# Kernel tuning notes

Hardware: AMD Instinct MI355X
Metric: run time of the kernel (lower is better)

The kernel has to match this reference:

```python
import jax, jax.numpy as jnp
import numpy as np

B, T, S, L_SRC, V, H, E, AV = 16, 128, 192, 192, 30522, 768, 768, 200
L_ORG = L_SRC - 1
KEEP, DEL, STOP, PAD = 3, 4, 2, 0  # SP_IDS = [KEEP, DEL, INSERT, STOP, PAD, LEFT, RIGHT, MARK]


def lstm(x, Wih, Whh, bih, bhh):
    # x: [B, T, E] -> outputs [B, T, H]; PyTorch gate order i, f, g, o
    Bx = x.shape[0]
    Hh = Whh.shape[1]
    def step(carry, xt):
        h, c = carry
        g = xt @ Wih.T + bih + h @ Whh.T + bhh
        i, f, gg, o = jnp.split(g, 4, axis=-1)
        c = jax.nn.sigmoid(f) * c + jax.nn.sigmoid(i) * jnp.tanh(gg)
        h = jax.nn.sigmoid(o) * jnp.tanh(c)
        return (h, c), h
    h0 = jnp.zeros((Bx, Hh), x.dtype)
    _, hs = jax.lax.scan(step, (h0, h0), jnp.swapaxes(x, 0, 1))
    return jnp.swapaxes(hs, 0, 1)


def compute_counters(input_edits, org_ids):
    # Vectorized replica of the host-side numpy counter bookkeeping.
    # Emits the PRE-update counters used at each timestep t (updated with gold = input_edits[:, t+1]).
    Bx = input_edits.shape[0]
    golds = jnp.swapaxes(input_edits[:, 1:], 0, 1)  # [T-1, B]
    barange = jnp.arange(Bx)
    Lorg = org_ids.shape[1]
    def step(carry, g):
        cd, ci, ca = carry
        pre = (cd, ci, ca)
        cd2 = cd + ((g == KEEP) | (g == DEL)).astype(jnp.int32)
        alive = (g != DEL) & (g != STOP) & (g != PAD)
        ci2 = ci + alive.astype(jnp.int32)
        nxt = jnp.clip(ca + 1, 0, Lorg - 1)
        tok = org_ids[barange, nxt]
        cond = alive & (g != KEEP) & (ca + 1 < Lorg) & ((tok == 103) | (tok == 3) | (tok == 4))
        ca2 = jnp.where(cond, ca + 1, jnp.maximum(cd2, ca))
        return (cd2, ci2, ca2), pre
    z = jnp.zeros((Bx,), jnp.int32)
    _, (cds, cis, cas) = jax.lax.scan(step, (z, z, z), golds)
    return jnp.swapaxes(cds, 0, 1), jnp.swapaxes(cis, 0, 1), jnp.swapaxes(cas, 0, 1)  # each [B, T-1]


def setup_inputs():
    key = jax.random.key(0)
    ks = jax.random.split(key, 40)
    s = 0.02
    rn = lambda k, sh: jax.random.normal(k, sh, jnp.float32) * s
    inp = {
        "input_edits": jax.random.randint(ks[0], (B, T), 0, 12),
        "input_actions": jax.random.randint(ks[1], (B, T), 0, AV),
        "simp_sent": jax.random.randint(ks[2], (B, S), 0, V),
        "org_ids": jax.random.randint(ks[3], (B, L_ORG), 0, V),
        "encoder_outputs_org": jax.random.normal(ks[4], (B, L_SRC, H), jnp.float32),
        "emb": rn(ks[5], (V, E)),
    }
    i = 6
    for nm in ("e", "a", "w"):
        inp["Wih_" + nm] = rn(ks[i], (4 * H, E)); i += 1
        inp["Whh_" + nm] = rn(ks[i], (4 * H, H)); i += 1
        inp["bih_" + nm] = jnp.zeros((4 * H,), jnp.float32)
        inp["bhh_" + nm] = jnp.zeros((4 * H,), jnp.float32)
    inp["W_align"] = rn(ks[i], (H, H)); i += 1
    inp["W_proj"] = rn(ks[i], (H, H)); i += 1
    inp["W_ref"] = rn(ks[i], (2, H)); i += 1
    inp["b_ref"] = jnp.zeros((2,), jnp.float32)
    inp["W_mlp"] = rn(ks[i], (E, 5 * H)); i += 1
    inp["b_mlp"] = jnp.zeros((E,), jnp.float32)
    inp["W_act"] = rn(ks[i], (E, 5 * H)); i += 1
    inp["b_act"] = jnp.zeros((E,), jnp.float32)
    inp["W_out"] = rn(ks[i], (V, E)); i += 1
    inp["b_out"] = jnp.zeros((V,), jnp.float32)
    inp["W_outact"] = rn(ks[i], (AV, E)); i += 1
    inp["b_outact"] = jnp.zeros((AV,), jnp.float32)
    m = np.full((1, AV), -100000.0, dtype=np.float32)
    m[0, [0, 1, 2, 5, 101, 102]] = 0.0
    inp["action_mask"] = jnp.asarray(m)
    return inp


def reference(input_edits, input_actions, simp_sent, org_ids, encoder_outputs_org, emb,
              Wih_e, Whh_e, bih_e, bhh_e, Wih_a, Whh_a, bih_a, bhh_a, Wih_w, Whh_w, bih_w, bhh_w,
              W_align, W_proj, W_ref, b_ref, W_mlp, b_mlp, W_act, b_act,
              W_out, b_out, W_outact, b_outact, action_mask):
    # tanh(output_hidden_alignment(enc)) then drop the first (CLS) position
    enc = jnp.tanh(encoder_outputs_org @ W_align.T)[:, 1:]  # [B, L_ORG, H]
    out_e = lstm(emb[input_edits], Wih_e, Whh_e, bih_e, bhh_e)
    out_a = lstm(emb[input_actions], Wih_a, Whh_a, bih_a, bhh_a)
    out_w = lstm(emb[simp_sent], Wih_w, Whh_w, bih_w, bhh_w)
    cd, ci, ca = compute_counters(input_edits, org_ids)  # [B, T-1] each
    Tm1 = input_edits.shape[1] - 1
    bidx = jnp.arange(enc.shape[0])[:, None]
    c_input = enc[bidx, cd]   # [B, T-1, H] data-dependent gather per timestep
    c_anno = enc[bidx, ca]
    c_word = out_w[bidx, ci]
    dec_e = out_e[:, :Tm1]
    dec_a = out_a[:, :Tm1]
    c_pair = jnp.stack([c_input, c_anno], axis=2)  # [B, T-1, 2, H]
    wref_e = jax.nn.softmax(dec_e @ W_ref.T + b_ref, axis=-1)
    wref_a = jax.nn.softmax(dec_a @ W_ref.T + b_ref, axis=-1)
    c_edit = jnp.einsum('btk,btkh->bth', wref_e, c_pair)
    c_action = jnp.einsum('btk,btkh->bth', wref_a, c_pair)
    attn = jax.nn.softmax(jnp.einsum('bth,blh->btl', c_word @ W_proj.T, enc), axis=-1)
    applied = jnp.einsum('btl,blh->bth', attn, enc)
    feat_a = jnp.concatenate([dec_a, dec_e, applied, c_action, c_word], axis=-1)
    act_log = jax.nn.log_softmax(jnp.tanh(feat_a @ W_act.T + b_act) @ W_outact.T + b_outact + action_mask[0], axis=-1)
    feat_e = jnp.concatenate([dec_e, dec_a, applied, c_edit, c_word], axis=-1)
    edit_log = jax.nn.log_softmax(jnp.tanh(feat_e @ W_mlp.T + b_mlp) @ W_out.T + b_out, axis=-1)
    return edit_log, act_log
```

## Files before the change

kernel.cpp:

```cpp
#include <hip/hip_runtime.h>
#include <hip/hip_bf16.h>

typedef __hip_bfloat16 bf16;

#define B_    16
#define T_    128
#define S_    192
#define H_    768
#define G4_   3072
#define V_    30522
#define AV_   200
#define L_    191
#define TM1_  127
#define R_    2032
#define K5_   3840
#define NB_   48
#define HSL_  16

typedef short bf16x8_t __attribute__((ext_vector_type(8)));
typedef float f32x4_t  __attribute__((ext_vector_type(4)));

__device__ __forceinline__ float bf2f(bf16 v) { return __bfloat162float(v); }
__device__ __forceinline__ bf16  f2bf(float v) { return __float2bfloat16(v); }
__device__ __forceinline__ unsigned short f2us(float v) { bf16 h = f2bf(v); return *reinterpret_cast<unsigned short*>(&h); }
__device__ __forceinline__ float uslo(unsigned u) { union { unsigned i; float f; } x; x.i = u << 16; return x.f; }
__device__ __forceinline__ float ushi(unsigned u) { union { unsigned i; float f; } x; x.i = u & 0xffff0000u; return x.f; }
__device__ __forceinline__ float us2f(unsigned short u) { union { unsigned i; float f; } x; x.i = ((unsigned)u) << 16; return x.f; }
__device__ __forceinline__ float sigm(float x) { return 1.0f / (1.0f + expf(-x)); }

__device__ __forceinline__ bf16x8_t ld8bf(const bf16* p) { return *(const bf16x8_t*)p; }
__device__ __forceinline__ bf16x8_t ld8bf(const float* p) {
    float4 a = *(const float4*)p;
    float4 b = *(const float4*)(p + 4);
    bf16x8_t r;
    r[0] = (short)f2us(a.x); r[1] = (short)f2us(a.y); r[2] = (short)f2us(a.z); r[3] = (short)f2us(a.w);
    r[4] = (short)f2us(b.x); r[5] = (short)f2us(b.y); r[6] = (short)f2us(b.z); r[7] = (short)f2us(b.w);
    return r;
}

template <typename TA, typename TW>
__global__ __launch_bounds__(256) void gemm_mfma(
    const TA* __restrict__ A, const TW* __restrict__ W,
    const float* __restrict__ bias1, const float* __restrict__ bias2,
    bf16* __restrict__ Ch, float* __restrict__ Cf,
    int M, int N, int K, int act, int rowdiv, int lda)
{
    __shared__ short As[128][40];
    __shared__ short Ws[128][40];
    const int tid = threadIdx.x;
    const int wave = tid >> 6, lane = tid & 63;
    const int mw = (wave >> 1) * 64, nw = (wave & 1) * 64;
    const int bm = blockIdx.x * 128, bn = blockIdx.y * 128;

    const int sr = tid >> 2;
    const int sc = (tid & 3) * 8;

    f32x4_t acc[4][4];
#pragma unroll
    for (int mi = 0; mi < 4; ++mi)
#pragma unroll
        for (int ni = 0; ni < 4; ++ni) acc[mi][ni] = (f32x4_t){0.f, 0.f, 0.f, 0.f};

    const int fr = lane & 15;
    const int fk = (lane >> 4) * 8;

    for (int k0 = 0; k0 < K; k0 += 32) {
#pragma unroll
        for (int c = 0; c < 2; ++c) {
            const int row = sr + c * 64;
            int ga = bm + row; if (ga > M - 1) ga = M - 1;
            const int ra = (rowdiv > 0) ? (ga + ga / rowdiv + 1) : ga;
            *(bf16x8_t*)&As[row][sc] = ld8bf(A + (size_t)ra * lda + k0 + sc);
            int gw = bn + row; if (gw > N - 1) gw = N - 1;
            *(bf16x8_t*)&Ws[row][sc] = ld8bf(W + (size_t)gw * K + k0 + sc);
        }
        __syncthreads();
        bf16x8_t af[4], wf[4];
#pragma unroll
        for (int i = 0; i < 4; ++i) af[i] = *(const bf16x8_t*)&As[mw + i * 16 + fr][fk];
#pragma unroll
        for (int i = 0; i < 4; ++i) wf[i] = *(const bf16x8_t*)&Ws[nw + i * 16 + fr][fk];
#pragma unroll
        for (int mi = 0; mi < 4; ++mi)
#pragma unroll
            for (int ni = 0; ni < 4; ++ni)
                acc[mi][ni] = __builtin_amdgcn_mfma_f32_16x16x32_bf16(af[mi], wf[ni], acc[mi][ni], 0, 0, 0);
        __syncthreads();
    }

    const int cl = lane & 15;
    const int rg = (lane >> 4) * 4;
#pragma unroll
    for (int mi = 0; mi < 4; ++mi) {
#pragma unroll
        for (int ni = 0; ni < 4; ++ni) {
            const int col = bn + nw + ni * 16 + cl;
            if (col >= N) continue;
#pragma unroll
            for (int j = 0; j < 4; ++j) {
                const int row = bm + mw + mi * 16 + rg + j;
                if (row >= M) continue;
                float v = acc[mi][ni][j];
                if (bias1) v += bias1[col];
                if (bias2) v += bias2[col];
                if (act == 1) v = tanhf(v);
                if (Ch) Ch[(size_t)row * N + col] = f2bf(v);
                else    Cf[(size_t)row * N + col] = v;
            }
        }
    }
}

__global__ void f2b_kernel(const float* __restrict__ in, bf16* __restrict__ out, int n4)
{
    const int i = blockIdx.x * 256 + threadIdx.x;
    if (i >= n4) return;
    float4 v = *(const float4*)(in + (size_t)i * 4);
    ushort4 o;
    o.x = f2us(v.x); o.y = f2us(v.y); o.z = f2us(v.z); o.w = f2us(v.w);
    *(ushort4*)(out + (size_t)i * 4) = o;
}

__global__ __launch_bounds__(256) void lstm_mfma_kernel(
    const bf16* __restrict__ pxe, const bf16* __restrict__ pxa, const bf16* __restrict__ pxw,
    const float* __restrict__ We, const float* __restrict__ Wa, const float* __restrict__ Ww,
    bf16* __restrict__ oute, bf16* __restrict__ outa, bf16* __restrict__ outw,
    unsigned short* __restrict__ hbuf, int* __restrict__ flags)
{
    const int which = blockIdx.x / NB_;
    const int nb = blockIdx.x % NB_;
    const bf16* px; const float* W; bf16* out; int Tn;
    if (which == 0)      { px = pxe; W = We; out = oute; Tn = T_; }
    else if (which == 1) { px = pxa; W = Wa; out = outa; Tn = T_; }
    else                 { px = pxw; W = Ww; out = outw; Tn = S_; }
    unsigned short* hG = hbuf + (size_t)which * (2 * B_ * H_);
    int* flg = flags + which * 64;

    const int tid = threadIdx.x;
    const int wv = tid >> 6;
    const int lane = tid & 63;
    const int so = nb * HSL_;

    __shared__ unsigned short hL[16][776];
    __shared__ float gS[4][16][17];
    __shared__ unsigned short oring[8][16][16];

    bf16x8_t Afrag[24];
    {
        const int m = lane & 15;
        const int kb8 = (lane >> 4) * 8;
        const float* wrow = W + (size_t)(wv * H_ + so + m) * H_ + kb8;
#pragma unroll
        for (int kb = 0; kb < 24; ++kb) {
            float4 f0 = *(const float4*)(wrow + kb * 32);
            float4 f1 = *(const float4*)(wrow + kb * 32 + 4);
            bf16x8_t a;
            a[0] = (short)f2us(f0.x); a[1] = (short)f2us(f0.y);
            a[2] = (short)f2us(f0.z); a[3] = (short)f2us(f0.w);
            a[4] = (short)f2us(f1.x); a[5] = (short)f2us(f1.y);
            a[6] = (short)f2us(f1.z); a[7] = (short)f2us(f1.w);
            Afrag[kb] = a;
        }
    }

    for (int i = tid; i < 16 * 776; i += 256) ((unsigned short*)hL)[i] = 0;

    const int cb = tid >> 4;
    const int chl = tid & 15;
    float c = 0.f;

    const int bn = lane & 15;
    const int bk = (lane >> 4) * 8;

    unsigned short pxr0, pxr1, pxr2, pxr3;
    {
        const bf16* q = px + ((size_t)cb * Tn + 0) * G4_ + so + chl;
        pxr0 = *(const unsigned short*)(q);
        pxr1 = *(const unsigned short*)(q + H_);
        pxr2 = *(const unsigned short*)(q + 2 * H_);
        pxr3 = *(const unsigned short*)(q + 3 * H_);
    }

    int cur = 0;
    for (int step = 0; step < Tn; ++step) {
        if (step > 0) {
            const unsigned long long* hsrc =
                (const unsigned long long*)(hG + (size_t)cur * (B_ * H_));
            for (int i = tid; i < B_ * H_ / 4; i += 256) {
                const unsigned long long v =
                    __hip_atomic_load(hsrc + i, __ATOMIC_RELAXED, __HIP_MEMORY_SCOPE_AGENT);
                const int bb = i / (H_ / 4);
                const int cc = i - bb * (H_ / 4);
                ((unsigned long long*)&hL[bb][0])[cc] = v;
            }
        }
        __syncthreads();

        f32x4_t acc = {0.f, 0.f, 0.f, 0.f};
#pragma unroll
        for (int kb = 0; kb < 24; ++kb) {
            bf16x8_t bfr = *(const bf16x8_t*)&hL[bn][kb * 32 + bk];
            acc = __builtin_amdgcn_mfma_f32_16x16x32_bf16(Afrag[kb], bfr, acc, 0, 0, 0);
        }
        {
            const int m0 = (lane >> 4) * 4;
#pragma unroll
            for (int j = 0; j < 4; ++j) gS[wv][m0 + j][bn] = acc[j];
        }
        __syncthreads();

        {
            const float gi = gS[0][chl][cb] + us2f(pxr0);
            const float gf = gS[1][chl][cb] + us2f(pxr1);
            const float gg = gS[2][chl][cb] + us2f(pxr2);
            const float go = gS[3][chl][cb] + us2f(pxr3);
            const float cn = sigm(gf) * c + sigm(gi) * tanhf(gg);
            const float hn = sigm(go) * tanhf(cn);
            c = cn;
            oring[step & 7][cb][chl] = f2us(hn);
            __hip_atomic_store(&hG[(size_t)(cur ^ 1) * (B_ * H_) + cb * H_ + so + chl],
                               f2us(hn), __ATOMIC_RELAXED, __HIP_MEMORY_SCOPE_AGENT);
        }

        if (step + 1 < Tn) {
            __syncthreads();
            const int target = step + 1;
            if (tid == 0)
                __hip_atomic_store(&flg[nb], target, __ATOMIC_RELAXED, __HIP_MEMORY_SCOPE_AGENT);
            {
                const bf16* q = px + ((size_t)cb * Tn + target) * G4_ + so + chl;
                pxr0 = *(const unsigned short*)(q);
                pxr1 = *(const unsigned short*)(q + H_);
                pxr2 = *(const unsigned short*)(q + 2 * H_);
                pxr3 = *(const unsigned short*)(q + 3 * H_);
            }
            if ((step & 7) == 7) {
                const int base = step & ~7;
                for (int s2 = 0; s2 < 8; ++s2)
                    out[((size_t)cb * Tn + base + s2) * H_ + so + chl] =
                        *reinterpret_cast<const bf16*>(&oring[s2][cb][chl]);
            }
            if (lane < NB_) {
                long guard = 0;
                while (__hip_atomic_load(&flg[lane], __ATOMIC_RELAXED, __HIP_MEMORY_SCOPE_AGENT) < target) {
                    __builtin_amdgcn_s_sleep(1);
                    if (++guard > 50000000L) break;
                }
            }
        } else {
            const int base = step & ~7;
            const int cnt8 = (step & 7) + 1;
            for (int s2 = 0; s2 < cnt8; ++s2)
                out[((size_t)cb * Tn + base + s2) * H_ + so + chl] =
                    *reinterpret_cast<const bf16*>(&oring[s2][cb][chl]);
        }
        cur ^= 1;
    }
}

__global__ void gather_rows_kernel(const int* __restrict__ ids,
                                   const float* __restrict__ emb,
                                   bf16* __restrict__ out)
{
    const int r = blockIdx.x;
    const float4* src = (const float4*)(emb + (size_t)ids[r] * H_);
    ushort4* dst = (ushort4*)(out + (size_t)r * H_);
    for (int h = threadIdx.x; h < H_ / 4; h += 256) {
        float4 v = src[h];
        ushort4 o;
        o.x = f2us(v.x); o.y = f2us(v.y); o.z = f2us(v.z); o.w = f2us(v.w);
        dst[h] = o;
    }
}

__global__ void counters_kernel(const int* __restrict__ edits, const int* __restrict__ org,
                                int* __restrict__ cd, int* __restrict__ ci, int* __restrict__ ca)
{
    const int b = threadIdx.x;
    if (b >= B_) return;
    int vd = 0, vi = 0, va = 0;
    for (int t = 0; t < TM1_; ++t) {
        cd[b * TM1_ + t] = vd; ci[b * TM1_ + t] = vi; ca[b * TM1_ + t] = va;
        const int g = edits[b * T_ + t + 1];
        const int vd2 = vd + ((g == 3 || g == 4) ? 1 : 0);
        const int alive = (g != 4 && g != 2 && g != 0) ? 1 : 0;
        const int vi2 = vi + alive;
        int nxt = va + 1; if (nxt > L_ - 1) nxt = L_ - 1;
        const int tok = org[b * L_ + nxt];
        const bool cond = alive && (g != 3) && (va + 1 < L_) && (tok == 103 || tok == 3 || tok == 4);
        const int va2 = cond ? (va + 1) : max(vd2, va);
        vd = vd2; vi = vi2; va = va2;
    }
}

__global__ void gather_cword_kernel(const bf16* __restrict__ outw, const int* __restrict__ ci,
                                    bf16* __restrict__ cw)
{
    const int r = blockIdx.x;
    const int b = r / TM1_;
    const unsigned* src = (const unsigned*)(outw + ((size_t)b * S_ + ci[r]) * H_);
    unsigned* dst = (unsigned*)(cw + (size_t)r * H_);
    for (int h = threadIdx.x; h < H_ / 2; h += 256) dst[h] = src[h];
}

__global__ __launch_bounds__(256) void ref_combine_kernel(
    const bf16* __restrict__ oute, const bf16* __restrict__ outa, const bf16* __restrict__ enc,
    const float* __restrict__ Wref, const float* __restrict__ bref,
    const int* __restrict__ cd, const int* __restrict__ ca,
    bf16* __restrict__ ced, bf16* __restrict__ cac)
{
    const int r = blockIdx.x;
    const int b = r / TM1_;
    const int t = r % TM1_;
    const bf16* de = oute + ((size_t)b * T_ + t) * H_;
    const bf16* da = outa + ((size_t)b * T_ + t) * H_;
    const int tid = threadIdx.x;
    __shared__ float red[256][4];
    float s0 = 0.f, s1 = 0.f, s2 = 0.f, s3 = 0.f;
    for (int k = tid; k < H_; k += 256) {
        const float w0 = Wref[k];
        const float w1 = Wref[H_ + k];
        const float e = bf2f(de[k]);
        const float a = bf2f(da[k]);
        s0 += e * w0; s1 += e * w1; s2 += a * w0; s3 += a * w1;
    }
    red[tid][0] = s0; red[tid][1] = s1; red[tid][2] = s2; red[tid][3] = s3;
    __syncthreads();
    for (int off = 128; off > 0; off >>= 1) {
        if (tid < off) {
            red[tid][0] += red[tid + off][0];
            red[tid][1] += red[tid + off][1];
            red[tid][2] += red[tid + off][2];
            red[tid][3] += red[tid + off][3];
        }
        __syncthreads();
    }
    const float br0 = bref[0], br1 = bref[1];
    const float xe0 = red[0][0] + br0, xe1 = red[0][1] + br1;
    const float xa0 = red[0][2] + br0, xa1 = red[0][3] + br1;
    const float me = fmaxf(xe0, xe1);
    const float ee0 = expf(xe0 - me), ee1 = expf(xe1 - me);
    const float pe0 = ee0 / (ee0 + ee1), pe1 = ee1 / (ee0 + ee1);
    const float ma = fmaxf(xa0, xa1);
    const float ea0 = expf(xa0 - ma), ea1 = expf(xa1 - ma);
    const float pa0 = ea0 / (ea0 + ea1), pa1 = ea1 / (ea0 + ea1);

    const bf16* ei = enc + ((size_t)b * L_ + cd[r]) * H_;
    const bf16* ea = enc + ((size_t)b * L_ + ca[r]) * H_;
    for (int h = tid; h < H_; h += 256) {
        const float vi = bf2f(ei[h]);
        const float va = bf2f(ea[h]);
        ced[(size_t)r * H_ + h] = f2bf(pe0 * vi + pe1 * va);
        cac[(size_t)r * H_ + h] = f2bf(pa0 * vi + pa1 * va);
    }
}

__global__ __launch_bounds__(256) void attn_kernel(const bf16* __restrict__ q,
                                                   const bf16* __restrict__ enc,
                                                   bf16* __restrict__ app)
{
    const int r = blockIdx.x;
    const int b = r / TM1_;
    const int tid = threadIdx.x;
    __shared__ float qs[H_];
    __shared__ float p[L_ + 1];
    __shared__ float red[256];
    const bf16* qrow = q + (size_t)r * H_;
    for (int h = tid; h < H_; h += 256) qs[h] = bf2f(qrow[h]);
    __syncthreads();
    const bf16* eb = enc + (size_t)b * L_ * H_;
    float myv = -1e30f;
    if (tid < L_) {
        const unsigned* er = (const unsigned*)(eb + (size_t)tid * H_);
        float s = 0.f;
        for (int k2 = 0; k2 < H_ / 2; ++k2) {
            const unsigned u = er[k2];
            s += qs[2 * k2] * uslo(u) + qs[2 * k2 + 1] * ushi(u);
        }
        p[tid] = s;
        myv = s;
    }
    red[tid] = myv;
    __syncthreads();
    for (int off = 128; off > 0; off >>= 1) {
        if (tid < off) red[tid] = fmaxf(red[tid], red[tid + off]);
        __syncthreads();
    }
    const float m = red[0];
    __syncthreads();
    float e = 0.f;
    if (tid < L_) e = expf(p[tid] - m);
    red[tid] = e;
    __syncthreads();
    for (int off = 128; off > 0; off >>= 1) {
        if (tid < off) red[tid] += red[tid + off];
        __syncthreads();
    }
    const float invZ = 1.f / red[0];
    __syncthreads();
    if (tid < L_) p[tid] = e * invZ;
    __syncthreads();
    for (int h = tid; h < H_; h += 256) {
        float s = 0.f;
        for (int l = 0; l < L_; ++l) s += p[l] * bf2f(eb[(size_t)l * H_ + h]);
        app[(size_t)r * H_ + h] = f2bf(s);
    }
}

__global__ void feat_kernel(const bf16* __restrict__ oute, const bf16* __restrict__ outa,
                            const bf16* __restrict__ app, const bf16* __restrict__ ced,
                            const bf16* __restrict__ cac, const bf16* __restrict__ cw,
                            bf16* __restrict__ fe, bf16* __restrict__ fa)
{
    const int r = blockIdx.x;
    const int b = r / TM1_;
    const int t = r % TM1_;
    const unsigned* de  = (const unsigned*)(oute + ((size_t)b * T_ + t) * H_);
    const unsigned* da  = (const unsigned*)(outa + ((size_t)b * T_ + t) * H_);
    const unsigned* ap  = (const unsigned*)(app + (size_t)r * H_);
    const unsigned* ce  = (const unsigned*)(ced + (size_t)r * H_);
    const unsigned* cA  = (const unsigned*)(cac + (size_t)r * H_);
    const unsigned* cwp = (const unsigned*)(cw + (size_t)r * H_);
    unsigned* pfe = (unsigned*)(fe + (size_t)r * K5_);
    unsigned* pfa = (unsigned*)(fa + (size_t)r * K5_);
    const int HW = H_ / 2;
    for (int h = threadIdx.x; h < HW; h += 256) {
        const unsigned ve = de[h], va = da[h], vap = ap[h], vce = ce[h], vca = cA[h], vcw = cwp[h];
        pfe[h] = ve;  pfe[HW + h] = va;  pfe[2 * HW + h] = vap; pfe[3 * HW + h] = vce; pfe[4 * HW + h] = vcw;
        pfa[h] = va;  pfa[HW + h] = ve;  pfa[2 * HW + h] = vap; pfa[3 * HW + h] = vca; pfa[4 * HW + h] = vcw;
    }
}

__global__ __launch_bounds__(1024) void logsoftmax_edit_kernel(float* __restrict__ out)
{
    float* row = out + (size_t)blockIdx.x * V_;
    const int tid = threadIdx.x;
    const int lane = tid & 63;
    const int wid = tid >> 6;
    __shared__ unsigned short rowb[V_];
    __shared__ float wredm[16], wreds[16];
    __shared__ float fin;

    float m = -1e30f, s = 0.f;
    for (int i = tid; i < V_; i += 1024) {
        const float x = row[i];
        rowb[i] = f2us(x);
        if (x > m) { s = s * expf(m - x) + 1.f; m = x; }
        else s += expf(x - m);
    }
#pragma unroll
    for (int off = 32; off > 0; off >>= 1) {
        const float m2 = __shfl_down(m, off);
        const float s2 = __shfl_down(s, off);
        const float mn = fmaxf(m, m2);
        s = s * expf(m - mn) + s2 * expf(m2 - mn);
        m = mn;
    }
    if (lane == 0) { wredm[wid] = m; wreds[wid] = s; }
    __syncthreads();
    if (wid == 0) {
        m = (lane < 16) ? wredm[lane] : -1e30f;
        s = (lane < 16) ? wreds[lane] : 0.f;
#pragma unroll
        for (int off = 8; off > 0; off >>= 1) {
            const float m2 = __shfl_down(m, off);
            const float s2 = __shfl_down(s, off);
            const float mn = fmaxf(m, m2);
            s = s * expf(m - mn) + s2 * expf(m2 - mn);
            m = mn;
        }
        if (lane == 0) fin = m + logf(s);
    }
    __syncthreads();
    const float lz = fin;
    for (int i = tid; i < V_; i += 1024) row[i] = us2f(rowb[i]) - lz;
}

__global__ __launch_bounds__(256) void logsoftmax_act_kernel(const float* __restrict__ in,
                                                             float* __restrict__ out)
{
    const float* row = in + (size_t)blockIdx.x * AV_;
    float* orow = out + (size_t)blockIdx.x * AV_;
    const int tid = threadIdx.x;
    __shared__ float red[256];
    float m = -1e30f;
    if (tid < AV_) m = row[tid];
    red[tid] = m;
    __syncthreads();
    for (int off = 128; off > 0; off >>= 1) {
        if (tid < off) red[tid] = fmaxf(red[tid], red[tid + off]);
        __syncthreads();
    }
    m = red[0];
    __syncthreads();
    float s = 0.f;
    if (tid < AV_) s = expf(row[tid] - m);
    red[tid] = s;
    __syncthreads();
    for (int off = 128; off > 0; off >>= 1) {
        if (tid < off) red[tid] += red[tid + off];
        __syncthreads();
    }
    const float lz = m + logf(red[0]);
    if (tid < AV_) orow[tid] = row[tid] - lz;
}

extern "C" void kernel_launch(void* const* d_in, const int* in_sizes, int n_in,
                              void* d_out, int out_size, void* d_ws, size_t ws_size,
                              hipStream_t stream)
{
    const int* input_edits   = (const int*)d_in[0];
    const int* input_actions = (const int*)d_in[1];
    const int* simp_sent     = (const int*)d_in[2];
    const int* org_ids       = (const int*)d_in[3];
    const float* enc_org     = (const float*)d_in[4];
    const float* emb         = (const float*)d_in[5];
    const float* Wih_e = (const float*)d_in[6];
    const float* Whh_e = (const float*)d_in[7];
    const float* bih_e = (const float*)d_in[8];
    const float* bhh_e = (const float*)d_in[9];
    const float* Wih_a = (const float*)d_in[10];
    const float* Whh_a = (const float*)d_in[11];
    const float* bih_a = (const float*)d_in[12];
    const float* bhh_a = (const float*)d_in[13];
    const float* Wih_w = (const float*)d_in[14];
    const float* Whh_w = (const float*)d_in[15];
    const float* bih_w = (const float*)d_in[16];
    const float* bhh_w = (const float*)d_in[17];
    const float* W_align = (const float*)d_in[18];
    const float* W_proj  = (const float*)d_in[19];
    const float* W_ref   = (const float*)d_in[20];
    const float* b_ref   = (const float*)d_in[21];
    const float* W_mlp   = (const float*)d_in[22];
    const float* b_mlp   = (const float*)d_in[23];
    const float* W_act   = (const float*)d_in[24];
    const float* b_act   = (const float*)d_in[25];
    const float* W_out   = (const float*)d_in[26];
    const float* b_out   = (const float*)d_in[27];
    const float* W_outact = (const float*)d_in[28];
    const float* b_outact = (const float*)d_in[29];
    const float* action_mask = (const float*)d_in[30];

    float* out = (float*)d_out;
    float* edit_out = out;
    float* act_out  = out + (size_t)R_ * V_;

    char* p = (char*)d_ws;
    auto take = [&](size_t bytes) { void* q = (void*)p; p += ((bytes + 255) / 256) * 256; return q; };
    int* flags = (int*)take(3 * 256);
    unsigned short* hbuf = (unsigned short*)take((size_t)3 * 2 * B_ * H_ * 2);
    char* alias_base = p;
    bf16* xe   = (bf16*)take((size_t)B_ * T_ * H_ * 2);
    bf16* xa   = (bf16*)take((size_t)B_ * T_ * H_ * 2);
    bf16* xw   = (bf16*)take((size_t)B_ * S_ * H_ * 2);
    bf16* pxe  = (bf16*)take((size_t)B_ * T_ * G4_ * 2);
    bf16* pxa  = (bf16*)take((size_t)B_ * T_ * G4_ * 2);
    bf16* pxw  = (bf16*)take((size_t)B_ * S_ * G4_ * 2);
    bf16* oute = (bf16*)take((size_t)B_ * T_ * H_ * 2);
    bf16* outa = (bf16*)take((size_t)B_ * T_ * H_ * 2);
    bf16* outw = (bf16*)take((size_t)B_ * S_ * H_ * 2);
    bf16* enc  = (bf16*)take((size_t)B_ * L_ * H_ * 2);
    bf16* cw   = (bf16*)take((size_t)R_ * H_ * 2);
    bf16* ced  = (bf16*)take((size_t)R_ * H_ * 2);
    bf16* cac  = (bf16*)take((size_t)R_ * H_ * 2);
    bf16* qb   = (bf16*)take((size_t)R_ * H_ * 2);
    bf16* app  = (bf16*)take((size_t)R_ * H_ * 2);
    bf16* fe   = (bf16*)take((size_t)R_ * K5_ * 2);
    bf16* fa   = (bf16*)take((size_t)R_ * K5_ * 2);
    bf16* he   = (bf16*)take((size_t)R_ * H_ * 2);
    bf16* ha   = (bf16*)take((size_t)R_ * H_ * 2);
    int*  cd   = (int*)take((size_t)R_ * 4);
    int*  ci   = (int*)take((size_t)R_ * 4);
    int*  ca   = (int*)take((size_t)R_ * 4);
    float* actbuf = (float*)take((size_t)R_ * AV_ * 4);
    bf16* Wob = (bf16*)alias_base;

    hipMemsetAsync(flags, 0, 3 * 256, stream);

    gather_rows_kernel<<<B_ * T_, 256, 0, stream>>>(input_edits, emb, xe);
    gather_rows_kernel<<<B_ * T_, 256, 0, stream>>>(input_actions, emb, xa);
    gather_rows_kernel<<<B_ * S_, 256, 0, stream>>>(simp_sent, emb, xw);

    dim3 gpx((B_ * T_ + 127) / 128, (G4_ + 127) / 128);
    gemm_mfma<bf16, float><<<gpx, 256, 0, stream>>>(xe, Wih_e, bih_e, bhh_e, pxe, nullptr, B_ * T_, G4_, H_, 0, 0, H_);
    gemm_mfma<bf16, float><<<gpx, 256, 0, stream>>>(xa, Wih_a, bih_a, bhh_a, pxa, nullptr, B_ * T_, G4_, H_, 0, 0, H_);
    dim3 gpxw((B_ * S_ + 127) / 128, (G4_ + 127) / 128);
    gemm_mfma<bf16, float><<<gpxw, 256, 0, stream>>>(xw, Wih_w, bih_w, bhh_w, pxw, nullptr, B_ * S_, G4_, H_, 0, 0, H_);

    dim3 genc((B_ * L_ + 127) / 128, (H_ + 127) / 128);
    gemm_mfma<float, float><<<genc, 256, 0, stream>>>(enc_org, W_align, nullptr, nullptr, enc, nullptr, B_ * L_, H_, H_, 1, L_, H_);

    counters_kernel<<<1, 64, 0, stream>>>(input_edits, org_ids, cd, ci, ca);

    lstm_mfma_kernel<<<3 * NB_, 256, 0, stream>>>(pxe, pxa, pxw, Whh_e, Whh_a, Whh_w,
                                                  oute, outa, outw, hbuf, flags);

    const int nW4 = V_ * H_ / 4;
    f2b_kernel<<<(nW4 + 255) / 256, 256, 0, stream>>>(W_out, Wob, nW4);

    gather_cword_kernel<<<R_, 256, 0, stream>>>(outw, ci, cw);

    ref_combine_kernel<<<R_, 256, 0, stream>>>(oute, outa, enc, W_ref, b_ref, cd, ca, ced, cac);

    dim3 gproj((R_ + 127) / 128, (H_ + 127) / 128);
    gemm_mfma<bf16, float><<<gproj, 256, 0, stream>>>(cw, W_proj, nullptr, nullptr, qb, nullptr, R_, H_, H_, 0, 0, H_);

    attn_kernel<<<R_, 256, 0, stream>>>(qb, enc, app);

    feat_kernel<<<R_, 256, 0, stream>>>(oute, outa, app, ced, cac, cw, fe, fa);

    gemm_mfma<bf16, float><<<gproj, 256, 0, stream>>>(fe, W_mlp, b_mlp, nullptr, he, nullptr, R_, H_, K5_, 1, 0, K5_);
    gemm_mfma<bf16, float><<<gproj, 256, 0, stream>>>(fa, W_act, b_act, nullptr, ha, nullptr, R_, H_, K5_, 1, 0, K5_);

    dim3 gact((R_ + 127) / 128, (AV_ + 127) / 128);
    gemm_mfma<bf16, float><<<gact, 256, 0, stream>>>(ha, W_outact, b_outact, action_mask, nullptr, actbuf, R_, AV_, H_, 0, 0, H_);
    logsoftmax_act_kernel<<<R_, 256, 0, stream>>>(actbuf, act_out);

    dim3 gedit((R_ + 127) / 128, (V_ + 127) / 128);
    gemm_mfma<bf16, bf16><<<gedit, 256, 0, stream>>>(he, Wob, b_out, nullptr, nullptr, edit_out, R_, V_, H_, 0, 0, H_);
    logsoftmax_edit_kernel<<<R_, 1024, 0, stream>>>(edit_out);
}
```

Measured before the change: 2.441 ms.

## Overlap W_out conversion with LSTM, pre-convert Wih, merge gathers, widen GEMM K tile

The fp32 W_out to bf16 conversion now runs on 96 extra blocks inside the persistent LSTM kernel, so it overlaps the latency-bound recurrence instead of running as a separate pass. The three Wih matrices are converted to bf16 once, in one launch, so the input-projection GEMMs load bf16 weights directly. The three embedding gathers become one launch, and the generic GEMM now stages a K tile of 64 per barrier instead of 32. Risks: the extra blocks in the LSTM launch compete for CUs and memory bandwidth with the spin-waiting recurrent blocks, and the larger shared-memory tiles may lower occupancy.

```diff
diff --git a/kernel.cpp b/kernel.cpp
--- a/kernel.cpp
+++ b/kernel.cpp
@@ -16,6 +16,7 @@
 #define K5_   3840
 #define NB_   48
 #define HSL_  16
+#define NCV_  96
 
 typedef short bf16x8_t __attribute__((ext_vector_type(8)));
 typedef float f32x4_t  __attribute__((ext_vector_type(4)));
@@ -45,15 +46,15 @@
     bf16* __restrict__ Ch, float* __restrict__ Cf,
     int M, int N, int K, int act, int rowdiv, int lda)
 {
-    __shared__ short As[128][40];
-    __shared__ short Ws[128][40];
+    __shared__ short As[128][72];
+    __shared__ short Ws[128][72];
     const int tid = threadIdx.x;
     const int wave = tid >> 6, lane = tid & 63;
     const int mw = (wave >> 1) * 64, nw = (wave & 1) * 64;
     const int bm = blockIdx.x * 128, bn = blockIdx.y * 128;
 
     const int sr = tid >> 2;
-    const int sc = (tid & 3) * 8;
+    const int sc = (tid & 3) * 16;
 
     f32x4_t acc[4][4];
 #pragma unroll
@@ -64,27 +65,40 @@
     const int fr = lane & 15;
     const int fk = (lane >> 4) * 8;
 
-    for (int k0 = 0; k0 < K; k0 += 32) {
-#pragma unroll
-        for (int c = 0; c < 2; ++c) {
-            const int row = sr + c * 64;
-            int ga = bm + row; if (ga > M - 1) ga = M - 1;
-            const int ra = (rowdiv > 0) ? (ga + ga / rowdiv + 1) : ga;
-            *(bf16x8_t*)&As[row][sc] = ld8bf(A + (size_t)ra * lda + k0 + sc);
-            int gw = bn + row; if (gw > N - 1) gw = N - 1;
-            *(bf16x8_t*)&Ws[row][sc] = ld8bf(W + (size_t)gw * K + k0 + sc);
-        }
-        __syncthreads();
-        bf16x8_t af[4], wf[4];
-#pragma unroll
-        for (int i = 0; i < 4; ++i) af[i] = *(const bf16x8_t*)&As[mw + i * 16 + fr][fk];
-#pragma unroll
-        for (int i = 0; i < 4; ++i) wf[i] = *(const bf16x8_t*)&Ws[nw + i * 16 + fr][fk];
-#pragma unroll
-        for (int mi = 0; mi < 4; ++mi)
-#pragma unroll
-            for (int ni = 0; ni < 4; ++ni)
-                acc[mi][ni] = __builtin_amdgcn_mfma_f32_16x16x32_bf16(af[mi], wf[ni], acc[mi][ni], 0, 0, 0);
+    int ga0 = bm + sr;       if (ga0 > M - 1) ga0 = M - 1;
+    int ga1 = bm + sr + 64;  if (ga1 > M - 1) ga1 = M - 1;
+    const int ra0 = (rowdiv > 0) ? (ga0 + ga0 / rowdiv + 1) : ga0;
+    const int ra1 = (rowdiv > 0) ? (ga1 + ga1 / rowdiv + 1) : ga1;
+    int gw0 = bn + sr;       if (gw0 > N - 1) gw0 = N - 1;
+    int gw1 = bn + sr + 64;  if (gw1 > N - 1) gw1 = N - 1;
+    const TA* aRow0 = A + (size_t)ra0 * lda;
+    const TA* aRow1 = A + (size_t)ra1 * lda;
+    const TW* wRow0 = W + (size_t)gw0 * K;
+    const TW* wRow1 = W + (size_t)gw1 * K;
+
+    for (int k0 = 0; k0 < K; k0 += 64) {
+#pragma unroll
+        for (int j = 0; j < 2; ++j) {
+            *(bf16x8_t*)&As[sr][sc + j * 8]      = ld8bf(aRow0 + k0 + sc + j * 8);
+            *(bf16x8_t*)&As[sr + 64][sc + j * 8] = ld8bf(aRow1 + k0 + sc + j * 8);
+            *(bf16x8_t*)&Ws[sr][sc + j * 8]      = ld8bf(wRow0 + k0 + sc + j * 8);
+            *(bf16x8_t*)&Ws[sr + 64][sc + j * 8] = ld8bf(wRow1 + k0 + sc + j * 8);
+        }
+        __syncthreads();
+#pragma unroll
+        for (int half = 0; half < 2; ++half) {
+            const int cb0 = half * 32 + fk;
+            bf16x8_t af[4], wf[4];
+#pragma unroll
+            for (int i = 0; i < 4; ++i) af[i] = *(const bf16x8_t*)&As[mw + i * 16 + fr][cb0];
+#pragma unroll
+            for (int i = 0; i < 4; ++i) wf[i] = *(const bf16x8_t*)&Ws[nw + i * 16 + fr][cb0];
+#pragma unroll
+            for (int mi = 0; mi < 4; ++mi)
+#pragma unroll
+                for (int ni = 0; ni < 4; ++ni)
+                    acc[mi][ni] = __builtin_amdgcn_mfma_f32_16x16x32_bf16(af[mi], wf[ni], acc[mi][ni], 0, 0, 0);
+        }
         __syncthreads();
     }
 
@@ -111,22 +125,43 @@
     }
 }
 
-__global__ void f2b_kernel(const float* __restrict__ in, bf16* __restrict__ out, int n4)
-{
+__global__ void conv3_kernel(const float* __restrict__ a, const float* __restrict__ b,
+                             const float* __restrict__ c,
+                             bf16* __restrict__ oa, bf16* __restrict__ ob,
+                             bf16* __restrict__ oc, int n4)
+{
+    const int which = blockIdx.y;
+    const float* src = (which == 0) ? a : (which == 1) ? b : c;
+    bf16* dst = (which == 0) ? oa : (which == 1) ? ob : oc;
     const int i = blockIdx.x * 256 + threadIdx.x;
     if (i >= n4) return;
-    float4 v = *(const float4*)(in + (size_t)i * 4);
+    float4 v = *(const float4*)(src + (size_t)i * 4);
     ushort4 o;
     o.x = f2us(v.x); o.y = f2us(v.y); o.z = f2us(v.z); o.w = f2us(v.w);
-    *(ushort4*)(out + (size_t)i * 4) = o;
+    *(ushort4*)(dst + (size_t)i * 4) = o;
 }
 
 __global__ __launch_bounds__(256) void lstm_mfma_kernel(
     const bf16* __restrict__ pxe, const bf16* __restrict__ pxa, const bf16* __restrict__ pxw,
     const float* __restrict__ We, const float* __restrict__ Wa, const float* __restrict__ Ww,
     bf16* __restrict__ oute, bf16* __restrict__ outa, bf16* __restrict__ outw,
-    unsigned short* __restrict__ hbuf, int* __restrict__ flags)
-{
+    unsigned short* __restrict__ hbuf, int* __restrict__ flags,
+    const float* __restrict__ Wout, bf16* __restrict__ Wob)
+{
+    const int tid = threadIdx.x;
+
+    if (blockIdx.x >= 3 * NB_) {
+        const int wid = blockIdx.x - 3 * NB_;
+        const int n4 = V_ * H_ / 4;
+        for (int i = wid * 256 + tid; i < n4; i += NCV_ * 256) {
+            float4 v = *(const float4*)(Wout + (size_t)i * 4);
+            ushort4 o;
+            o.x = f2us(v.x); o.y = f2us(v.y); o.z = f2us(v.z); o.w = f2us(v.w);
+            *(ushort4*)(Wob + (size_t)i * 4) = o;
+        }
+        return;
+    }
+
     const int which = blockIdx.x / NB_;
     const int nb = blockIdx.x % NB_;
     const bf16* px; const float* W; bf16* out; int Tn;
@@ -136,7 +171,6 @@
     unsigned short* hG = hbuf + (size_t)which * (2 * B_ * H_);
     int* flg = flags + which * 64;
 
-    const int tid = threadIdx.x;
     const int wv = tid >> 6;
     const int lane = tid & 63;
     const int so = nb * HSL_;
@@ -258,11 +292,18 @@
     }
 }
 
-__global__ void gather_rows_kernel(const int* __restrict__ ids,
-                                   const float* __restrict__ emb,
-                                   bf16* __restrict__ out)
-{
+__global__ void gather3_kernel(const int* __restrict__ ids_e, const int* __restrict__ ids_a,
+                               const int* __restrict__ ids_w, const float* __restrict__ emb,
+                               bf16* __restrict__ oe, bf16* __restrict__ oa,
+                               bf16* __restrict__ ow)
+{
+    const int which = blockIdx.y;
     const int r = blockIdx.x;
+    const int* ids; bf16* out; int nr;
+    if (which == 0)      { ids = ids_e; out = oe; nr = B_ * T_; }
+    else if (which == 1) { ids = ids_a; out = oa; nr = B_ * T_; }
+    else                 { ids = ids_w; out = ow; nr = B_ * S_; }
+    if (r >= nr) return;
     const float4* src = (const float4*)(emb + (size_t)ids[r] * H_);
     ushort4* dst = (ushort4*)(out + (size_t)r * H_);
     for (int h = threadIdx.x; h < H_ / 4; h += 256) {
@@ -574,29 +615,33 @@
     int*  ca   = (int*)take((size_t)R_ * 4);
     float* actbuf = (float*)take((size_t)R_ * AV_ * 4);
     bf16* Wob = (bf16*)alias_base;
+    bf16* WihEb = fe;
+    bf16* WihAb = fe + (size_t)G4_ * H_;
+    bf16* WihWb = fe + (size_t)2 * G4_ * H_;
 
     hipMemsetAsync(flags, 0, 3 * 256, stream);
 
-    gather_rows_kernel<<<B_ * T_, 256, 0, stream>>>(input_edits, emb, xe);
-    gather_rows_kernel<<<B_ * T_, 256, 0, stream>>>(input_actions, emb, xa);
-    gather_rows_kernel<<<B_ * S_, 256, 0, stream>>>(simp_sent, emb, xw);
+    const int nW4i = G4_ * H_ / 4;
+    conv3_kernel<<<dim3((nW4i + 255) / 256, 3), 256, 0, stream>>>(
+        Wih_e, Wih_a, Wih_w, WihEb, WihAb, WihWb, nW4i);
+
+    gather3_kernel<<<dim3(B_ * S_, 3), 256, 0, stream>>>(
+        input_edits, input_actions, simp_sent, emb, xe, xa, xw);
 
     dim3 gpx((B_ * T_ + 127) / 128, (G4_ + 127) / 128);
-    gemm_mfma<bf16, float><<<gpx, 256, 0, stream>>>(xe, Wih_e, bih_e, bhh_e, pxe, nullptr, B_ * T_, G4_, H_, 0, 0, H_);
-    gemm_mfma<bf16, float><<<gpx, 256, 0, stream>>>(xa, Wih_a, bih_a, bhh_a, pxa, nullptr, B_ * T_, G4_, H_, 0, 0, H_);
+    gemm_mfma<bf16, bf16><<<gpx, 256, 0, stream>>>(xe, WihEb, bih_e, bhh_e, pxe, nullptr, B_ * T_, G4_, H_, 0, 0, H_);
+    gemm_mfma<bf16, bf16><<<gpx, 256, 0, stream>>>(xa, WihAb, bih_a, bhh_a, pxa, nullptr, B_ * T_, G4_, H_, 0, 0, H_);
     dim3 gpxw((B_ * S_ + 127) / 128, (G4_ + 127) / 128);
-    gemm_mfma<bf16, float><<<gpxw, 256, 0, stream>>>(xw, Wih_w, bih_w, bhh_w, pxw, nullptr, B_ * S_, G4_, H_, 0, 0, H_);
+    gemm_mfma<bf16, bf16><<<gpxw, 256, 0, stream>>>(xw, WihWb, bih_w, bhh_w, pxw, nullptr, B_ * S_, G4_, H_, 0, 0, H_);
 
     dim3 genc((B_ * L_ + 127) / 128, (H_ + 127) / 128);
     gemm_mfma<float, float><<<genc, 256, 0, stream>>>(enc_org, W_align, nullptr, nullptr, enc, nullptr, B_ * L_, H_, H_, 1, L_, H_);
 
     counters_kernel<<<1, 64, 0, stream>>>(input_edits, org_ids, cd, ci, ca);
 
-    lstm_mfma_kernel<<<3 * NB_, 256, 0, stream>>>(pxe, pxa, pxw, Whh_e, Whh_a, Whh_w,
-                                                  oute, outa, outw, hbuf, flags);
-
-    const int nW4 = V_ * H_ / 4;
-    f2b_kernel<<<(nW4 + 255) / 256, 256, 0, stream>>>(W_out, Wob, nW4);
+    lstm_mfma_kernel<<<3 * NB_ + NCV_, 256, 0, stream>>>(pxe, pxa, pxw, Whh_e, Whh_a, Whh_w,
+                                                         oute, outa, outw, hbuf, flags,
+                                                         W_out, Wob);
 
     gather_cword_kernel<<<R_, 256, 0, stream>>>(outw, ci, cw);
 
```

Result: faster. 2.208 ms (-9.5%).
